# Kernel optimization log

Measured on AMD Instinct MI355X. Metric: run time of the kernel, lower is better.

Reference implementation:

```python
import jax, jax.numpy as jnp
import numpy as np

FRAME_LEN = 256
HOP = 128
T_WINDOW = 128
N_MELS = 64


def setup_inputs() -> dict:
    key = jax.random.key(0)
    x_raw = jax.random.normal(key, (32, 16, 160000), dtype=jnp.float32)
    return {"x_raw": x_raw}


def reference(x_raw):
    # TF stft with pad_end=True: num_frames = ceil(T / hop)
    t = x_raw.shape[-1]
    num_frames = -(-t // HOP)
    pad = (num_frames - 1) * HOP + FRAME_LEN - t
    xp = jnp.pad(x_raw, ((0, 0), (0, 0), (0, pad)))

    # periodic Hann window (tf.signal.hann_window default)
    n = jnp.arange(FRAME_LEN, dtype=jnp.float32)
    window = 0.5 - 0.5 * jnp.cos(2.0 * jnp.pi * n / FRAME_LEN)

    # frame all batch/sensor signals at once: [B, S, F, L]
    idx = jnp.arange(num_frames)[:, None] * HOP + jnp.arange(FRAME_LEN)[None, :]
    frames = xp[..., idx] * window

    # batched real FFT -> [B, S, F, FRAME_LEN//2 + 1]
    stft = jnp.fft.rfft(frames, n=FRAME_LEN, axis=-1)
    logmag = jnp.log(jnp.abs(stft) + 1e-9)
    norm = jnp.clip(logmag, -12.0, 12.0)

    # tf.image.resize bilinear (half-pixel centers, no antialias)
    B, S = norm.shape[0], norm.shape[1]
    out = jax.image.resize(norm, (B, S, T_WINDOW, N_MELS), method="bilinear", antialias=False)
    return jnp.clip(out, -12.0, 12.0)
```

## Files before the change

### kernel.cpp

```cpp
#include <hip/hip_runtime.h>
#include <math.h>

#define HOP     128
#define SIGLEN  160000
#define NWAVES  4096
#define GITER   4
#define TWO_PI  6.2831853071795864f

__device__ __forceinline__ float2 pk_add(float2 a, float2 b) {
    float2 d; asm("v_pk_add_f32 %0, %1, %2" : "=v"(d) : "v"(a), "v"(b)); return d;
}
__device__ __forceinline__ float2 pk_sub(float2 a, float2 b) {
    float2 d; asm("v_pk_add_f32 %0, %1, %2 neg_lo:[0,1] neg_hi:[0,1]" : "=v"(d) : "v"(a), "v"(b)); return d;
}
__device__ __forceinline__ float2 pk_add_neghi(float2 a, float2 b) {
    float2 d; asm("v_pk_add_f32 %0, %1, %2 neg_hi:[0,1]" : "=v"(d) : "v"(a), "v"(b)); return d;
}

__device__ __forceinline__ float2 cmul(float2 a, float2 b) {
    float2 m, r;
    asm("v_pk_mul_f32 %0, %1, %2 op_sel:[1,1] op_sel_hi:[0,1] neg_lo:[1,0]"
        : "=v"(m) : "v"(a), "v"(b));
    asm("v_pk_fma_f32 %0, %1, %2, %3 op_sel:[0,0,0] op_sel_hi:[1,0,1]"
        : "=v"(r) : "v"(a), "v"(b), "v"(m));
    return r;
}
__device__ __forceinline__ float2 cmul_mi(float2 a) {
    return make_float2(a.y, -a.x);
}

__device__ __forceinline__ void r4c(float2 a, float2 b, float2 c, float2 d,
                                    float2& y0, float2& y1, float2& y2, float2& y3) {
    float2 t0 = pk_add(a, c), t1 = pk_sub(a, c);
    float2 t2 = pk_add(b, d), t3 = pk_sub(b, d);
    y0 = pk_add(t0, t2);
    y2 = pk_sub(t0, t2);
    asm("v_pk_add_f32 %0, %1, %2 op_sel:[0,1] op_sel_hi:[1,0] neg_hi:[0,1]"
        : "=v"(y1) : "v"(t1), "v"(t3));
    asm("v_pk_add_f32 %0, %1, %2 op_sel:[0,1] op_sel_hi:[1,0] neg_lo:[0,1]"
        : "=v"(y3) : "v"(t1), "v"(t3));
}

__device__ __forceinline__ void dft16(const float2* p, float2* q) {
    float2 u[4][4];
    #pragma unroll
    for (int b = 0; b < 4; ++b)
        r4c(p[b], p[4 + b], p[8 + b], p[12 + b], u[0][b], u[1][b], u[2][b], u[3][b]);
    const float C  = 0.70710678118654752f;
    const float c1 = 0.92387953251128676f, s1 = 0.38268343236508977f;
    u[1][1] = cmul(u[1][1], make_float2(c1, -s1));
    u[2][1] = cmul(u[2][1], make_float2(C, -C));
    u[3][1] = cmul(u[3][1], make_float2(s1, -c1));
    u[1][2] = cmul(u[1][2], make_float2(C, -C));
    u[2][2] = cmul_mi(u[2][2]);
    u[3][2] = cmul(u[3][2], make_float2(-C, -C));
    u[1][3] = cmul(u[1][3], make_float2(s1, -c1));
    u[2][3] = cmul(u[2][3], make_float2(-C, -C));
    u[3][3] = cmul(u[3][3], make_float2(-c1, s1));
    #pragma unroll
    for (int c = 0; c < 4; ++c)
        r4c(u[c][0], u[c][1], u[c][2], u[c][3], q[c], q[c + 4], q[c + 8], q[c + 12]);
}

__device__ __forceinline__ float2 unpack_log(float2 A, float2 B) {
    float2 f0 = pk_add_neghi(A, B);
    float2 f1;
    asm("v_pk_add_f32 %0, %1, %2 op_sel:[1,1] op_sel_hi:[0,0] neg_hi:[1,0]"
        : "=v"(f1) : "v"(A), "v"(B));
    float p0 = f0.x * f0.x + f0.y * f0.y;
    float p1 = f1.x * f1.x + f1.y * f1.y;
    float l0 = 0.5f * __logf(p0) - 0.69314718f;
    float l1 = 0.5f * __logf(p1) - 0.69314718f;
    return make_float2(fminf(fmaxf(l0, -12.0f), 12.0f),
                       fminf(fmaxf(l1, -12.0f), 12.0f));
}

#define FENCE() asm volatile("" ::: "memory")

__global__ __launch_bounds__(64, 4) void spectro_kernel(const float* __restrict__ x,
                                                        float* __restrict__ out) {
    const int wv   = blockIdx.x;
    const int lane = threadIdx.x;
    const int row  = lane >> 4;
    const int n2   = lane & 15;

    __shared__ float2 lds[1092];
    float2* Lrow = lds + 273 * row;

    float  wtab8[8];
    float2 tw[8];
    #pragma unroll
    for (int i = 0; i < 8; ++i) {
        wtab8[i] = 0.5f - 0.5f * __cosf((float)(16 * i + n2) * (TWO_PI / 256.0f));
        float ang = (float)(n2 * (i + 1)) * (TWO_PI / 256.0f);
        tw[i] = make_float2(__cosf(ang), -__sinf(ang));
    }

    #pragma unroll 1
    for (int it = 0; it < GITER; ++it) {
        const int g   = GITER * wv + it;
        const int t   = 4 * (g & 31) + row;
        const int sig = g >> 5;
        const float src_t = ((float)t + 0.5f) * (1250.0f / 128.0f) - 0.5f;
        const int   t0 = (int)src_t;
        const float ft = src_t - (float)t0;
        const float* xb = x + (long)sig * SIGLEN + (long)t0 * HOP + n2;

        float cur[24];
        #pragma unroll
        for (int k = 0; k < 24; ++k) cur[k] = xb[16 * k];

        float2 z[16];
        #pragma unroll
        for (int n1 = 0; n1 < 16; ++n1) {
            float w = (n1 < 8) ? wtab8[n1] : 1.0f - wtab8[n1 - 8];
            z[n1] = make_float2(w * cur[n1], w * cur[n1 + 8]);
        }

        float2 A[16];
        dft16(z, A);
        #pragma unroll
        for (int k1 = 1; k1 < 16; ++k1) {
            if (k1 <= 8) A[k1] = cmul(A[k1], tw[k1 - 1]);
            else         A[k1] = cmul(cmul(A[k1], tw[7]), tw[k1 - 9]);
        }

        #pragma unroll
        for (int k1 = 0; k1 < 16; ++k1) Lrow[17 * k1 + n2] = A[k1];
        FENCE();
        float2 B[16];
        #pragma unroll
        for (int j = 0; j < 16; ++j) B[j] = Lrow[17 * n2 + j];
        FENCE();

        float2 X16[16];
        dft16(B, X16);
        #pragma unroll
        for (int k2 = 0; k2 < 16; ++k2) Lrow[16 * k2 + n2] = X16[k2];
        FENCE();

        #pragma unroll
        for (int j = 0; j < 4; ++j) {
            const int m = 16 * j + n2;
            const float src_m = ((float)m + 0.5f) * (129.0f / 64.0f) - 0.5f;
            const int   m0 = (int)src_m;
            const float fm = src_m - (float)m0;
            float2 A0 = Lrow[m0];
            float2 A1 = Lrow[m0 + 1];
            float2 B0 = Lrow[(256 - m0) & 255];
            float2 B1 = Lrow[255 - m0];
            float2 L0 = unpack_log(A0, B0);
            float2 L1 = unpack_log(A1, B1);
            float va = L0.x * (1.0f - fm) + L1.x * fm;
            float vb = L0.y * (1.0f - fm) + L1.y * fm;
            float val = va * (1.0f - ft) + vb * ft;
            val = fminf(fmaxf(val, -12.0f), 12.0f);
            out[(long)(4 * g + row) * 64 + m] = val;
        }
        FENCE();
    }
}

extern "C" void kernel_launch(void* const* d_in, const int* in_sizes, int n_in,
                              void* d_out, int out_size, void* d_ws, size_t ws_size,
                              hipStream_t stream) {
    const float* x = (const float*)d_in[0];
    float* out = (float*)d_out;
    spectro_kernel<<<dim3(NWAVES), dim3(64), 0, stream>>>(x, out);
}
```

Measured before the change: 28.57 us.

## Swizzle LDS FFT transpose layout with float4 stores and precomputed twiddles

Result: slower. 31.84 us (+11.4%).

```diff
diff --git a/kernel.cpp b/kernel.cpp
--- a/kernel.cpp
+++ b/kernel.cpp
@@ -26,7 +26,10 @@
     return r;
 }
 __device__ __forceinline__ float2 cmul_mi(float2 a) {
-    return make_float2(a.y, -a.x);
+    float2 d;
+    asm("v_pk_add_f32 %0, %1, 0 op_sel:[1,0] op_sel_hi:[0,1] neg_hi:[1,0]"
+        : "=v"(d) : "v"(a));
+    return d;
 }
 
 __device__ __forceinline__ void r4c(float2 a, float2 b, float2 c, float2 d,
@@ -84,17 +87,19 @@
     const int row  = lane >> 4;
     const int n2   = lane & 15;
 
-    __shared__ float2 lds[1092];
-    float2* Lrow = lds + 273 * row;
+    __shared__ float2 lds[1024];
+    float2* Lrow = lds + 256 * row;
 
     float  wtab8[8];
-    float2 tw[8];
+    float2 tw[15];
     #pragma unroll
     for (int i = 0; i < 8; ++i) {
         wtab8[i] = 0.5f - 0.5f * __cosf((float)(16 * i + n2) * (TWO_PI / 256.0f));
         float ang = (float)(n2 * (i + 1)) * (TWO_PI / 256.0f);
         tw[i] = make_float2(__cosf(ang), -__sinf(ang));
     }
+    #pragma unroll
+    for (int j = 9; j <= 15; ++j) tw[j - 1] = cmul(tw[7], tw[j - 9]);
 
     #pragma unroll 1
     for (int it = 0; it < GITER; ++it) {
@@ -120,23 +125,28 @@
         float2 A[16];
         dft16(z, A);
         #pragma unroll
-        for (int k1 = 1; k1 < 16; ++k1) {
-            if (k1 <= 8) A[k1] = cmul(A[k1], tw[k1 - 1]);
-            else         A[k1] = cmul(cmul(A[k1], tw[7]), tw[k1 - 9]);
-        }
+        for (int k1 = 1; k1 < 16; ++k1) A[k1] = cmul(A[k1], tw[k1 - 1]);
 
         #pragma unroll
-        for (int k1 = 0; k1 < 16; ++k1) Lrow[17 * k1 + n2] = A[k1];
+        for (int p = 0; p < 8; ++p) {
+            const int u = 16 * n2 + ((2 * p + 2 * n2) & 15);
+            *(float4*)(&Lrow[u]) = make_float4(A[2 * p].x, A[2 * p].y,
+                                               A[2 * p + 1].x, A[2 * p + 1].y);
+        }
         FENCE();
         float2 B[16];
         #pragma unroll
-        for (int j = 0; j < 16; ++j) B[j] = Lrow[17 * n2 + j];
+        for (int j = 0; j < 16; ++j) B[j] = Lrow[16 * j + ((n2 + 2 * j) & 15)];
         FENCE();
 
         float2 X16[16];
         dft16(B, X16);
         #pragma unroll
-        for (int k2 = 0; k2 < 16; ++k2) Lrow[16 * k2 + n2] = X16[k2];
+        for (int q = 0; q < 8; ++q) {
+            const int u = 16 * n2 + ((2 * q + 2 * n2) & 15);
+            *(float4*)(&Lrow[u]) = make_float4(X16[2 * q].x, X16[2 * q].y,
+                                               X16[2 * q + 1].x, X16[2 * q + 1].y);
+        }
         FENCE();
 
         #pragma unroll
@@ -145,15 +155,17 @@
             const float src_m = ((float)m + 0.5f) * (129.0f / 64.0f) - 0.5f;
             const int   m0 = (int)src_m;
             const float fm = src_m - (float)m0;
-            float2 A0 = Lrow[m0];
-            float2 A1 = Lrow[m0 + 1];
-            float2 B0 = Lrow[(256 - m0) & 255];
-            float2 B1 = Lrow[255 - m0];
+            const int ba = m0, bb = m0 + 1;
+            const int bc = (256 - m0) & 255, bd = 255 - m0;
+            float2 A0 = Lrow[16 * (ba & 15) + (((ba >> 4) + 2 * (ba & 15)) & 15)];
+            float2 A1 = Lrow[16 * (bb & 15) + (((bb >> 4) + 2 * (bb & 15)) & 15)];
+            float2 B0 = Lrow[16 * (bc & 15) + (((bc >> 4) + 2 * (bc & 15)) & 15)];
+            float2 B1 = Lrow[16 * (bd & 15) + (((bd >> 4) + 2 * (bd & 15)) & 15)];
             float2 L0 = unpack_log(A0, B0);
             float2 L1 = unpack_log(A1, B1);
-            float va = L0.x * (1.0f - fm) + L1.x * fm;
-            float vb = L0.y * (1.0f - fm) + L1.y * fm;
-            float val = va * (1.0f - ft) + vb * ft;
+            float va = L0.x + fm * (L1.x - L0.x);
+            float vb = L0.y + fm * (L1.y - L0.y);
+            float val = va + ft * (vb - va);
             val = fminf(fmaxf(val, -12.0f), 12.0f);
             out[(long)(4 * g + row) * 64 + m] = val;
         }
```
